# Kernel tuning notes

Hardware: AMD Instinct MI355X
Metric: run time of the kernel (lower is better)

## Reference

```python
import jax, jax.numpy as jnp
import numpy as np

N_NODES = 50000
N_EDGES = 800000
N_FEAT = 64
N_HID = 64
N_CLASSES = 10
N_GRAPHS = 64


def setup_inputs() -> dict:
    key = jax.random.key(0)
    ks = jax.random.split(key, 14)
    # edge_index with no self-loops (PyG add_remaining_self_loops then appends
    # exactly one self loop per node, which the reference reproduces)
    row = jax.random.randint(ks[0], (N_EDGES,), 0, N_NODES, dtype=jnp.int32)
    off = jax.random.randint(ks[1], (N_EDGES,), 1, N_NODES, dtype=jnp.int32)
    col = (row + off) % N_NODES
    edge_index = jnp.stack([row, col])
    batch = jnp.sort(jax.random.randint(ks[2], (N_NODES,), 0, N_GRAPHS, dtype=jnp.int32))
    x = jax.random.normal(ks[3], (N_NODES, N_FEAT), jnp.float32)
    P_vec = jax.random.normal(ks[4], (N_EDGES,), jnp.float32)

    def lin(k, fi, fo):
        return jax.random.normal(k, (fi, fo), jnp.float32) * (1.0 / np.sqrt(fi))

    return {
        "x": x, "edge_index": edge_index, "batch": batch, "P_vec": P_vec,
        "W1": lin(ks[5], N_FEAT, N_HID), "b1": jax.random.normal(ks[6], (N_HID,)) * 0.02,
        "W2": lin(ks[7], N_HID, N_HID), "b2": jax.random.normal(ks[8], (N_HID,)) * 0.02,
        "W3": lin(ks[9], N_HID, N_HID), "b3": jax.random.normal(ks[10], (N_HID,)) * 0.02,
        "Wl": lin(ks[11], N_HID, N_CLASSES), "bl": jax.random.normal(ks[12], (N_CLASSES,)) * 0.02,
    }


def reference(x, edge_index, batch, P_vec, W1, b1, W2, b2, W3, b3, Wl, bl):
    n = x.shape[0]
    row, col = edge_index[0], edge_index[1]
    # add_remaining_self_loops: append one self loop per node with weight 1.0
    sl = jnp.arange(n, dtype=row.dtype)
    fr = jnp.concatenate([row, sl])          # [E+N] source
    fc = jnp.concatenate([col, sl])          # [E+N] target (flow source_to_target)
    w = jnp.concatenate([jax.nn.sigmoid(P_vec), jnp.ones((n,), x.dtype)])
    deg = jax.ops.segment_sum(w, fc, num_segments=n)
    dis = jnp.where(deg > 0, deg ** -0.5, 0.0)  # deg_inv_sqrt, inf->0
    norm = dis[fr] * w * dis[fc]             # identical for all 3 conv layers

    def gcn_layer(h, W, b):
        h = h @ W                             # Linear (no bias inside lin)
        agg = jax.ops.segment_sum(norm[:, None] * h[fr], fc, num_segments=n)
        return agg + b

    h = jax.nn.relu(gcn_layer(x, W1, b1))
    h = jax.nn.relu(gcn_layer(h, W2, b2))
    h = gcn_layer(h, W3, b3)
    # global_mean_pool over batch segment ids
    sums = jax.ops.segment_sum(h, batch, num_segments=N_GRAPHS)
    cnt = jax.ops.segment_sum(jnp.ones((n, 1), h.dtype), batch, num_segments=N_GRAPHS)
    pooled = sums / jnp.maximum(cnt, 1.0)
    # dropout is identity at inference; final classifier
    return pooled @ Wl + bl
```

## Files before the change

### kernel.cpp

```cpp
#include <hip/hip_runtime.h>
#include <hip/hip_bf16.h>
#include <hip/hip_fp16.h>
#include <math.h>

#define N_GRAPHS 64
#define N_CLASSES 10
#define FIXSCALE 262144.0f
#define MAXDEG 64

typedef __hip_bfloat16 bf16;

__device__ __forceinline__ unsigned int pack_edge(int r, float s) {
    return ((unsigned int)r << 16) | (unsigned int)__half_as_ushort(__float2half(s));
}

__global__ void init_k(unsigned int* __restrict__ packed,
                       float* __restrict__ sums, float* __restrict__ cntG, int n) {
    int i = blockIdx.x * 256 + threadIdx.x;
    if (i < n) packed[i] = 0u;
    if (i < N_GRAPHS * 64) sums[i] = 0.0f;
    if (i < N_GRAPHS) cntG[i] = 0.0f;
}

__global__ void hist_k(const float* __restrict__ P, const int* __restrict__ row,
                       const int* __restrict__ col,
                       unsigned int* __restrict__ packed,
                       unsigned int* __restrict__ ell, int E) {
    int e = blockIdx.x * 256 + threadIdx.x;
    if (e < E) {
        float s = 1.0f / (1.0f + expf(-P[e]));
        unsigned int v = (1u << 24) | (unsigned int)(s * FIXSCALE + 0.5f);
        unsigned int old = atomicAdd(&packed[col[e]], v);
        unsigned int rank = old >> 24;
        if (rank < MAXDEG) ell[col[e] * MAXDEG + rank] = pack_edge(row[e], s);
    }
}

__global__ void disxg_k(const unsigned int* __restrict__ packed,
                        const float* __restrict__ x,
                        float* __restrict__ dis, bf16* __restrict__ xg,
                        unsigned int* __restrict__ ell, int n) {
    int i = blockIdx.x * 256 + threadIdx.x;
    if (i < n * 64) {
        int node = i >> 6;
        int lane = i & 63;
        unsigned int pk = packed[node];
        float deg = 1.0f + (float)(pk & 0xFFFFFFu) * (1.0f / FIXSCALE);
        float dv = 1.0f / sqrtf(deg);
        xg[i] = __float2bfloat16(x[i] * dv);
        if (lane == 0) dis[node] = dv;
        int cnt = (int)(pk >> 24);
        if (cnt > MAXDEG) cnt = MAXDEG;
        int pad = ((cnt + 15) & ~15) - cnt;
        if (lane < pad) ell[node * MAXDEG + cnt + lane] = 0u;
    }
}

__global__ void fold_k(const float* __restrict__ W3, const float* __restrict__ b3,
                       const float* __restrict__ Wl, const float* __restrict__ bl,
                       float* __restrict__ Wc, float* __restrict__ bc) {
    int t = blockIdx.x * 256 + threadIdx.x;
    if (t < 64 * N_CLASSES) {
        int k = t / N_CLASSES, c = t % N_CLASSES;
        float acc = 0.0f;
        for (int m = 0; m < 64; ++m) acc += W3[k * 64 + m] * Wl[m * N_CLASSES + c];
        Wc[t] = acc;
    }
    if (t < N_CLASSES) {
        float acc = bl[t];
        for (int m = 0; m < 64; ++m) acc += b3[m] * Wl[m * N_CLASSES + t];
        bc[t] = acc;
    }
}

__device__ __forceinline__ float edge_term(unsigned int v, const bf16* g, int lane) {
    int r = (int)(v >> 16);
    float s = __half2float(__ushort_as_half((unsigned short)(v & 0xFFFFu)));
    return s * __bfloat162float(g[r * 64 + lane]);
}

template <int MODE>
__global__ __launch_bounds__(256) void agg_mm_k(const bf16* __restrict__ g,
                                                const unsigned int* __restrict__ ell,
                                                const unsigned int* __restrict__ packed,
                                                const float* __restrict__ dis,
                                                const float* __restrict__ W,
                                                const float* __restrict__ b,
                                                float* __restrict__ out,
                                                bf16* __restrict__ out_bf, int n) {
    __shared__ float Wlds[MODE ? 64 * 64 : 1];
    int tid = threadIdx.x;
    if (MODE == 1) {
        for (int i = tid; i < 64 * 64; i += 256) Wlds[i] = W[i];
        __syncthreads();
    }
    int node = __builtin_amdgcn_readfirstlane(blockIdx.x * 4 + (tid >> 6));
    if (node >= n) return;
    int lane = tid & 63;

    float bv = (MODE == 1) ? b[lane] : 0.0f;
    float d = dis[node];
    int cnt = (int)(packed[node] >> 24);
    if (cnt > MAXDEG) cnt = MAXDEG;
    int cnt16 = (cnt + 15) & ~15;
    float acc = __bfloat162float(g[node * 64 + lane]);
    const unsigned int* rowp = ell + node * MAXDEG;

    float a[16];
#pragma unroll
    for (int t = 0; t < 16; ++t) a[t] = 0.0f;
    for (int j = 0; j < cnt16; j += 16) {
        unsigned int v[16];
#pragma unroll
        for (int t = 0; t < 16; ++t) v[t] = rowp[j + t];
#pragma unroll
        for (int t = 0; t < 16; ++t) a[t] += edge_term(v[t], g, lane);
    }
#pragma unroll
    for (int off = 8; off >= 1; off >>= 1)
#pragma unroll
        for (int t = 0; t < off; ++t) a[t] += a[t + off];
    acc += a[0];
    acc *= d;

    if (MODE == 1) {
        float o0 = bv, o1 = 0.f, o2 = 0.f, o3 = 0.f;
#pragma unroll
        for (int k = 0; k < 64; k += 4) {
            float av0 = __int_as_float(__builtin_amdgcn_readlane(__float_as_int(acc), k));
            float av1 = __int_as_float(__builtin_amdgcn_readlane(__float_as_int(acc), k + 1));
            float av2 = __int_as_float(__builtin_amdgcn_readlane(__float_as_int(acc), k + 2));
            float av3 = __int_as_float(__builtin_amdgcn_readlane(__float_as_int(acc), k + 3));
            o0 = fmaf(av0, Wlds[(k + 0) * 64 + lane], o0);
            o1 = fmaf(av1, Wlds[(k + 1) * 64 + lane], o1);
            o2 = fmaf(av2, Wlds[(k + 2) * 64 + lane], o2);
            o3 = fmaf(av3, Wlds[(k + 3) * 64 + lane], o3);
        }
        float o = fmaxf((o0 + o1) + (o2 + o3), 0.0f);
        out_bf[node * 64 + lane] = __float2bfloat16(d * o);
    } else {
        out[node * 64 + lane] = acc;
    }
}

__global__ __launch_bounds__(256) void poolpart_k(const float* __restrict__ h,
                                                  const int* __restrict__ batch,
                                                  float* __restrict__ sums,
                                                  float* __restrict__ cntG, int n) {
    int wave = threadIdx.x >> 6, lane = threadIdx.x & 63;
    int base = blockIdx.x * 128 + wave * 32;
    if (base >= n) return;
    int end = base + 32; if (end > n) end = n;
    int g = batch[base];
    float acc = 0.0f;
    int run = 0;
    for (int i = base; i < end; ++i) {
        int gi = batch[i];
        if (gi != g) {
            atomicAdd(&sums[g * 64 + lane], acc);
            if (lane == 0) atomicAdd(&cntG[g], (float)run);
            g = gi; acc = 0.0f; run = 0;
        }
        acc += h[i * 64 + lane];
        ++run;
    }
    atomicAdd(&sums[g * 64 + lane], acc);
    if (lane == 0) atomicAdd(&cntG[g], (float)run);
}

__global__ void classify_k(const float* __restrict__ sums, const float* __restrict__ cntG,
                           const float* __restrict__ Wc, const float* __restrict__ bc,
                           float* __restrict__ out) {
    __shared__ float pooled[64];
    int g = blockIdx.x;
    int t = threadIdx.x;
    float inv = 1.0f / fmaxf(cntG[g], 1.0f);
    pooled[t] = sums[g * 64 + t] * inv;
    __syncthreads();
    if (t < N_CLASSES) {
        float acc = bc[t];
        for (int k = 0; k < 64; ++k) acc += pooled[k] * Wc[k * N_CLASSES + t];
        out[g * N_CLASSES + t] = acc;
    }
}

extern "C" void kernel_launch(void* const* d_in, const int* in_sizes, int n_in,
                              void* d_out, int out_size, void* d_ws, size_t ws_size,
                              hipStream_t stream) {
    const float* x     = (const float*)d_in[0];
    const int*   eidx  = (const int*)d_in[1];
    const int*   batch = (const int*)d_in[2];
    const float* P     = (const float*)d_in[3];
    const float* W1 = (const float*)d_in[4];
    const float* b1 = (const float*)d_in[5];
    const float* W2 = (const float*)d_in[6];
    const float* b2 = (const float*)d_in[7];
    const float* W3 = (const float*)d_in[8];
    const float* b3 = (const float*)d_in[9];
    const float* Wl = (const float*)d_in[10];
    const float* bl = (const float*)d_in[11];
    float* out = (float*)d_out;

    const int N = in_sizes[2];
    const int E = in_sizes[3];
    const int* row = eidx;
    const int* col = eidx + E;

    char* p = (char*)d_ws;
    unsigned int* packed = (unsigned int*)p; p += (size_t)N * 4;
    float* dis      = (float*)p; p += (size_t)N * 4;
    float* sums     = (float*)p; p += (size_t)N_GRAPHS * 64 * 4;
    float* cntG     = (float*)p; p += (size_t)N_GRAPHS * 4;
    float* Wc       = (float*)p; p += (size_t)64 * N_CLASSES * 4;
    float* bc       = (float*)p; p += (size_t)N_CLASSES * 4;
    unsigned int* ell = (unsigned int*)p; p += (size_t)N * MAXDEG * 4;
    float* bufF     = (float*)p; p += (size_t)N * 64 * 4;
    bf16*  xg       = (bf16*)p;  p += (size_t)N * 64 * 2;
    bf16*  gA       = (bf16*)p;  p += (size_t)N * 64 * 2;
    bf16*  gB       = xg;

    dim3 blk(256);
    int nodeG = (N + 255) / 256;
    int edgeG = (E + 255) / 256;
    int bigG  = (N * 64 + 255) / 256;

    init_k<<<nodeG, blk, 0, stream>>>(packed, sums, cntG, N);
    hist_k<<<edgeG, blk, 0, stream>>>(P, row, col, packed, ell, E);
    disxg_k<<<bigG, blk, 0, stream>>>(packed, x, dis, xg, ell, N);
    fold_k<<<(64 * N_CLASSES + 255) / 256, blk, 0, stream>>>(W3, b3, Wl, bl, Wc, bc);

    int aggG = (N + 3) / 4;

    agg_mm_k<1><<<aggG, blk, 0, stream>>>(xg, ell, packed, dis, W1, b1, nullptr, gA, N);
    agg_mm_k<1><<<aggG, blk, 0, stream>>>(gA, ell, packed, dis, W2, b2, nullptr, gB, N);
    agg_mm_k<0><<<aggG, blk, 0, stream>>>(gB, ell, packed, dis, nullptr, nullptr, bufF, nullptr, N);

    int poolG = (N + 127) / 128;
    poolpart_k<<<poolG, blk, 0, stream>>>(bufF, batch, sums, cntG, N);
    classify_k<<<N_GRAPHS, dim3(64), 0, stream>>>(sums, cntG, Wc, bc, out);
}
```

Baseline: 258.0 us.

## Process two nodes per wave in aggregation, recompute dis inline, fold fold_k into init

Each wavefront now aggregates two adjacent nodes together, interleaving their ELL gathers so more independent loads are in flight and sharing the LDS weight reads across both nodes in the matmul. ELL padding is extended to the larger 16-aligned count of each node pair so the shared loop bound stays valid. The dis array is dropped and recomputed from the packed degree in the aggregation kernels, and the weight-folding kernel is merged into init_k to save a launch. The cost is extra padded gathers when paired nodes differ in degree, plus higher register pressure.

Measured after the change: 261.9 us. About the same (+1.5%).

```diff
diff --git a/kernel.cpp b/kernel.cpp
--- a/kernel.cpp
+++ b/kernel.cpp
@@ -15,11 +15,25 @@
 }
 
 __global__ void init_k(unsigned int* __restrict__ packed,
-                       float* __restrict__ sums, float* __restrict__ cntG, int n) {
+                       float* __restrict__ sums, float* __restrict__ cntG,
+                       const float* __restrict__ W3, const float* __restrict__ b3,
+                       const float* __restrict__ Wl, const float* __restrict__ bl,
+                       float* __restrict__ Wc, float* __restrict__ bc, int n) {
     int i = blockIdx.x * 256 + threadIdx.x;
     if (i < n) packed[i] = 0u;
     if (i < N_GRAPHS * 64) sums[i] = 0.0f;
     if (i < N_GRAPHS) cntG[i] = 0.0f;
+    if (i < 64 * N_CLASSES) {
+        int k = i / N_CLASSES, c = i % N_CLASSES;
+        float acc = 0.0f;
+        for (int m = 0; m < 64; ++m) acc += W3[k * 64 + m] * Wl[m * N_CLASSES + c];
+        Wc[i] = acc;
+    }
+    if (i < N_CLASSES) {
+        float acc = bl[i];
+        for (int m = 0; m < 64; ++m) acc += b3[m] * Wl[m * N_CLASSES + i];
+        bc[i] = acc;
+    }
 }
 
 __global__ void hist_k(const float* __restrict__ P, const int* __restrict__ row,
@@ -37,8 +51,7 @@
 }
 
 __global__ void disxg_k(const unsigned int* __restrict__ packed,
-                        const float* __restrict__ x,
-                        float* __restrict__ dis, bf16* __restrict__ xg,
+                        const float* __restrict__ x, bf16* __restrict__ xg,
                         unsigned int* __restrict__ ell, int n) {
     int i = blockIdx.x * 256 + threadIdx.x;
     if (i < n * 64) {
@@ -48,42 +61,30 @@
         float deg = 1.0f + (float)(pk & 0xFFFFFFu) * (1.0f / FIXSCALE);
         float dv = 1.0f / sqrtf(deg);
         xg[i] = __float2bfloat16(x[i] * dv);
-        if (lane == 0) dis[node] = dv;
         int cnt = (int)(pk >> 24);
         if (cnt > MAXDEG) cnt = MAXDEG;
-        int pad = ((cnt + 15) & ~15) - cnt;
+        int partner = ((node ^ 1) < n) ? (node ^ 1) : node;
+        unsigned int pkp = packed[partner];
+        int cntp = (int)(pkp >> 24);
+        if (cntp > MAXDEG) cntp = MAXDEG;
+        int cA = (cnt + 15) & ~15, cB = (cntp + 15) & ~15;
+        int cmax = cA > cB ? cA : cB;
+        int pad = cmax - cnt;
         if (lane < pad) ell[node * MAXDEG + cnt + lane] = 0u;
     }
 }
 
-__global__ void fold_k(const float* __restrict__ W3, const float* __restrict__ b3,
-                       const float* __restrict__ Wl, const float* __restrict__ bl,
-                       float* __restrict__ Wc, float* __restrict__ bc) {
-    int t = blockIdx.x * 256 + threadIdx.x;
-    if (t < 64 * N_CLASSES) {
-        int k = t / N_CLASSES, c = t % N_CLASSES;
-        float acc = 0.0f;
-        for (int m = 0; m < 64; ++m) acc += W3[k * 64 + m] * Wl[m * N_CLASSES + c];
-        Wc[t] = acc;
-    }
-    if (t < N_CLASSES) {
-        float acc = bl[t];
-        for (int m = 0; m < 64; ++m) acc += b3[m] * Wl[m * N_CLASSES + t];
-        bc[t] = acc;
-    }
-}
-
-__device__ __forceinline__ float edge_term(unsigned int v, const bf16* g, int lane) {
-    int r = (int)(v >> 16);
-    float s = __half2float(__ushort_as_half((unsigned short)(v & 0xFFFFu)));
-    return s * __bfloat162float(g[r * 64 + lane]);
+__device__ __forceinline__ float rec_s(unsigned int v) {
+    return __half2float(__ushort_as_half((unsigned short)(v & 0xFFFFu)));
+}
+__device__ __forceinline__ float rl(float x, int k) {
+    return __int_as_float(__builtin_amdgcn_readlane(__float_as_int(x), k));
 }
 
 template <int MODE>
 __global__ __launch_bounds__(256) void agg_mm_k(const bf16* __restrict__ g,
                                                 const unsigned int* __restrict__ ell,
                                                 const unsigned int* __restrict__ packed,
-                                                const float* __restrict__ dis,
                                                 const float* __restrict__ W,
                                                 const float* __restrict__ b,
                                                 float* __restrict__ out,
@@ -94,52 +95,76 @@
         for (int i = tid; i < 64 * 64; i += 256) Wlds[i] = W[i];
         __syncthreads();
     }
-    int node = __builtin_amdgcn_readfirstlane(blockIdx.x * 4 + (tid >> 6));
-    if (node >= n) return;
+    int wid = __builtin_amdgcn_readfirstlane(blockIdx.x * 4 + (tid >> 6));
+    int n0 = wid * 2;
+    if (n0 >= n) return;
+    int n1 = n0 + 1;
+    bool has1 = (n1 < n);
+    int n1c = has1 ? n1 : n0;
     int lane = tid & 63;
-
     float bv = (MODE == 1) ? b[lane] : 0.0f;
-    float d = dis[node];
-    int cnt = (int)(packed[node] >> 24);
-    if (cnt > MAXDEG) cnt = MAXDEG;
-    int cnt16 = (cnt + 15) & ~15;
-    float acc = __bfloat162float(g[node * 64 + lane]);
-    const unsigned int* rowp = ell + node * MAXDEG;
-
-    float a[16];
-#pragma unroll
-    for (int t = 0; t < 16; ++t) a[t] = 0.0f;
-    for (int j = 0; j < cnt16; j += 16) {
-        unsigned int v[16];
-#pragma unroll
-        for (int t = 0; t < 16; ++t) v[t] = rowp[j + t];
-#pragma unroll
-        for (int t = 0; t < 16; ++t) a[t] += edge_term(v[t], g, lane);
-    }
-#pragma unroll
-    for (int off = 8; off >= 1; off >>= 1)
-#pragma unroll
-        for (int t = 0; t < off; ++t) a[t] += a[t + off];
-    acc += a[0];
-    acc *= d;
+
+    unsigned int pk0 = packed[n0];
+    unsigned int pk1 = packed[n1c];
+    float d0 = 1.0f / sqrtf(1.0f + (float)(pk0 & 0xFFFFFFu) * (1.0f / FIXSCALE));
+    float d1 = 1.0f / sqrtf(1.0f + (float)(pk1 & 0xFFFFFFu) * (1.0f / FIXSCALE));
+    int c0 = (int)(pk0 >> 24); if (c0 > MAXDEG) c0 = MAXDEG;
+    int c1 = has1 ? (int)(pk1 >> 24) : 0; if (c1 > MAXDEG) c1 = MAXDEG;
+    int cm = c0 > c1 ? c0 : c1;
+    int cmax = (cm + 15) & ~15;
+
+    float acc0 = __bfloat162float(g[n0 * 64 + lane]);
+    float acc1 = __bfloat162float(g[n1c * 64 + lane]);
+    const unsigned int* p0 = ell + (size_t)n0 * MAXDEG;
+    const unsigned int* p1 = ell + (size_t)n1c * MAXDEG;
+
+    float a0[8], a1[8];
+#pragma unroll
+    for (int t = 0; t < 8; ++t) { a0[t] = 0.0f; a1[t] = 0.0f; }
+    for (int j = 0; j < cmax; j += 8) {
+        unsigned int v0[8], v1[8];
+#pragma unroll
+        for (int t = 0; t < 8; ++t) v0[t] = p0[j + t];
+#pragma unroll
+        for (int t = 0; t < 8; ++t) v1[t] = p1[j + t];
+        float w0[8], w1[8];
+#pragma unroll
+        for (int t = 0; t < 8; ++t) w0[t] = __bfloat162float(g[(v0[t] >> 16) * 64 + lane]);
+#pragma unroll
+        for (int t = 0; t < 8; ++t) w1[t] = __bfloat162float(g[(v1[t] >> 16) * 64 + lane]);
+#pragma unroll
+        for (int t = 0; t < 8; ++t) a0[t] = fmaf(rec_s(v0[t]), w0[t], a0[t]);
+#pragma unroll
+        for (int t = 0; t < 8; ++t) a1[t] = fmaf(rec_s(v1[t]), w1[t], a1[t]);
+    }
+#pragma unroll
+    for (int off = 4; off >= 1; off >>= 1)
+#pragma unroll
+        for (int t = 0; t < off; ++t) { a0[t] += a0[t + off]; a1[t] += a1[t + off]; }
+    acc0 = (acc0 + a0[0]) * d0;
+    acc1 = (acc1 + a1[0]) * d1;
 
     if (MODE == 1) {
         float o0 = bv, o1 = 0.f, o2 = 0.f, o3 = 0.f;
+        float q0 = bv, q1 = 0.f, q2 = 0.f, q3 = 0.f;
 #pragma unroll
         for (int k = 0; k < 64; k += 4) {
-            float av0 = __int_as_float(__builtin_amdgcn_readlane(__float_as_int(acc), k));
-            float av1 = __int_as_float(__builtin_amdgcn_readlane(__float_as_int(acc), k + 1));
-            float av2 = __int_as_float(__builtin_amdgcn_readlane(__float_as_int(acc), k + 2));
-            float av3 = __int_as_float(__builtin_amdgcn_readlane(__float_as_int(acc), k + 3));
-            o0 = fmaf(av0, Wlds[(k + 0) * 64 + lane], o0);
-            o1 = fmaf(av1, Wlds[(k + 1) * 64 + lane], o1);
-            o2 = fmaf(av2, Wlds[(k + 2) * 64 + lane], o2);
-            o3 = fmaf(av3, Wlds[(k + 3) * 64 + lane], o3);
+            float wk0 = Wlds[(k + 0) * 64 + lane];
+            float wk1 = Wlds[(k + 1) * 64 + lane];
+            float wk2 = Wlds[(k + 2) * 64 + lane];
+            float wk3 = Wlds[(k + 3) * 64 + lane];
+            o0 = fmaf(rl(acc0, k + 0), wk0, o0); q0 = fmaf(rl(acc1, k + 0), wk0, q0);
+            o1 = fmaf(rl(acc0, k + 1), wk1, o1); q1 = fmaf(rl(acc1, k + 1), wk1, q1);
+            o2 = fmaf(rl(acc0, k + 2), wk2, o2); q2 = fmaf(rl(acc1, k + 2), wk2, q2);
+            o3 = fmaf(rl(acc0, k + 3), wk3, o3); q3 = fmaf(rl(acc1, k + 3), wk3, q3);
         }
-        float o = fmaxf((o0 + o1) + (o2 + o3), 0.0f);
-        out_bf[node * 64 + lane] = __float2bfloat16(d * o);
+        float oA = fmaxf((o0 + o1) + (o2 + o3), 0.0f);
+        float oB = fmaxf((q0 + q1) + (q2 + q3), 0.0f);
+        out_bf[n0 * 64 + lane] = __float2bfloat16(d0 * oA);
+        if (has1) out_bf[n1 * 64 + lane] = __float2bfloat16(d1 * oB);
     } else {
-        out[node * 64 + lane] = acc;
+        out[n0 * 64 + lane] = acc0;
+        if (has1) out[n1 * 64 + lane] = acc1;
     }
 }
 
@@ -208,7 +233,6 @@
 
     char* p = (char*)d_ws;
     unsigned int* packed = (unsigned int*)p; p += (size_t)N * 4;
-    float* dis      = (float*)p; p += (size_t)N * 4;
     float* sums     = (float*)p; p += (size_t)N_GRAPHS * 64 * 4;
     float* cntG     = (float*)p; p += (size_t)N_GRAPHS * 4;
     float* Wc       = (float*)p; p += (size_t)64 * N_CLASSES * 4;
@@ -224,16 +248,15 @@
     int edgeG = (E + 255) / 256;
     int bigG  = (N * 64 + 255) / 256;
 
-    init_k<<<nodeG, blk, 0, stream>>>(packed, sums, cntG, N);
+    init_k<<<nodeG, blk, 0, stream>>>(packed, sums, cntG, W3, b3, Wl, bl, Wc, bc, N);
     hist_k<<<edgeG, blk, 0, stream>>>(P, row, col, packed, ell, E);
-    disxg_k<<<bigG, blk, 0, stream>>>(packed, x, dis, xg, ell, N);
-    fold_k<<<(64 * N_CLASSES + 255) / 256, blk, 0, stream>>>(W3, b3, Wl, bl, Wc, bc);
-
-    int aggG = (N + 3) / 4;
-
-    agg_mm_k<1><<<aggG, blk, 0, stream>>>(xg, ell, packed, dis, W1, b1, nullptr, gA, N);
-    agg_mm_k<1><<<aggG, blk, 0, stream>>>(gA, ell, packed, dis, W2, b2, nullptr, gB, N);
-    agg_mm_k<0><<<aggG, blk, 0, stream>>>(gB, ell, packed, dis, nullptr, nullptr, bufF, nullptr, N);
+    disxg_k<<<bigG, blk, 0, stream>>>(packed, x, xg, ell, N);
+
+    int aggG = (N + 7) / 8;
+
+    agg_mm_k<1><<<aggG, blk, 0, stream>>>(xg, ell, packed, W1, b1, nullptr, gA, N);
+    agg_mm_k<1><<<aggG, blk, 0, stream>>>(gA, ell, packed, W2, b2, nullptr, gB, N);
+    agg_mm_k<0><<<aggG, blk, 0, stream>>>(gB, ell, packed, nullptr, nullptr, bufF, nullptr, N);
 
     int poolG = (N + 127) / 128;
     poolpart_k<<<poolG, blk, 0, stream>>>(bufF, batch, sums, cntG, N);
```
